# Performance work log

Hardware: AMD Instinct MI355X
Metric: run time of the kernel (lower is better)

## Reference

```python
import jax, jax.numpy as jnp
import numpy as np

SIGMA = 25.0
B = 4096            # number of graphs
N = 1048576         # total nodes across batch
FEAT = 44           # node feature dim
TED = 84            # t_embed_dim = 128 - 44


def setup_inputs() -> dict:
    key = jax.random.key(0)
    ks = jax.random.split(key, 12)
    # ragged graph sizes via sorted random cut points -> ptr of length B+1
    cuts = jnp.sort(jax.random.randint(ks[0], (B - 1,), 0, N))
    ptr = jnp.concatenate([jnp.zeros((1,), jnp.int32), cuts.astype(jnp.int32), jnp.full((1,), N, jnp.int32)])
    node_attr = jax.random.normal(ks[1], (N, FEAT), dtype=jnp.float32)
    t = jax.random.uniform(ks[2], (B,), dtype=jnp.float32, minval=1e-3, maxval=1.0)
    # GaussianFourierProjection buffer (requires_grad=False in torch)
    W_f = jax.random.normal(ks[3], (TED // 2,), dtype=jnp.float32) * 30.0
    # embed Linear 84->84
    embed_w = jax.random.normal(ks[4], (TED, TED), dtype=jnp.float32) / np.sqrt(TED)
    embed_b = jax.random.normal(ks[5], (TED,), dtype=jnp.float32) * 0.01
    # Linear chain 128->64->32->4 (torch convention: W [out, in])
    w0 = jax.random.normal(ks[6], (64, 128), dtype=jnp.float32) / np.sqrt(128)
    b0 = jax.random.normal(ks[7], (64,), dtype=jnp.float32) * 0.01
    w1 = jax.random.normal(ks[8], (32, 64), dtype=jnp.float32) / np.sqrt(64)
    b1 = jax.random.normal(ks[9], (32,), dtype=jnp.float32) * 0.01
    w2 = jax.random.normal(ks[10], (4, 32), dtype=jnp.float32) / np.sqrt(32)
    b2 = jax.random.normal(ks[11], (4,), dtype=jnp.float32) * 0.01
    return {"node_attr": node_attr, "t": t, "ptr": ptr, "W_f": W_f,
            "embed_w": embed_w, "embed_b": embed_b,
            "w0": w0, "b0": b0, "w1": w1, "b1": b1, "w2": w2, "b2": b2}


def reference(node_attr, t, ptr, W_f, embed_w, embed_b, w0, b0, w1, b1, w2, b2):
    swish = lambda x: x * jax.nn.sigmoid(x)
    # GaussianFourierProjection: [B, TED]
    x_proj = t[:, None] * W_f[None, :] * (2.0 * np.pi)
    t_emb = jnp.concatenate([jnp.sin(x_proj), jnp.cos(x_proj)], axis=-1)
    embed = swish(t_emb @ embed_w.T + embed_b)                      # [B, TED]
    # ragged broadcast: graph id per node (replaces the torch per-graph tile loop)
    seg = jnp.searchsorted(ptr, jnp.arange(node_attr.shape[0], dtype=ptr.dtype), side='right') - 1
    h = jnp.concatenate([node_attr, embed[seg]], axis=-1)           # [N, 128]
    h = swish(h @ w0.T + b0)                                        # [N, 64]
    h = swish(h @ w1.T + b1)                                        # [N, 32]
    h = swish(h @ w2.T + b2)                                        # [N, 4]
    std = jnp.sqrt((SIGMA ** (2.0 * t) - 1.0) / (2.0 * np.log(SIGMA)))  # [B]
    return h / std[seg][:, None]
```

## Files before the change

### kernel.cpp

```cpp
#include <hip/hip_runtime.h>
#include <hip/hip_fp16.h>

typedef _Float16 f16x8 __attribute__((ext_vector_type(8)));
typedef __fp16   fp16x2 __attribute__((ext_vector_type(2)));
typedef float f32x4 __attribute__((ext_vector_type(4)));

#define FEAT 44
#define TED  84
#define MT   128
#define WN   32
#define NBLK 768
#define BUFB 6144

__global__ void prep_all(const float* __restrict__ t_arr, const float* __restrict__ W_f,
                         const float* __restrict__ embed_w, const float* __restrict__ embed_b,
                         const float* __restrict__ w0, const float* __restrict__ b0,
                         const float* __restrict__ w1, const float* __restrict__ w2,
                         const int* __restrict__ gptr, int* __restrict__ seg, int do_seg,
                         float* __restrict__ emb0, float* __restrict__ inv_std,
                         _Float16* __restrict__ w0h, _Float16* __restrict__ w1h,
                         _Float16* __restrict__ w2h, int B) {
    int g   = blockIdx.x;
    int tid = threadIdx.x;
    if (g == B) {
        for (int i = tid; i < 64 * 64; i += 128) {
            int o = i >> 6, k = i & 63;
            w0h[i] = (k < FEAT) ? (_Float16)w0[o * 128 + k] : (_Float16)0.f;
        }
        for (int i = tid; i < 32 * 64; i += 128) w1h[i] = (_Float16)w1[i];
        for (int i = tid; i < 16 * 32; i += 128) w2h[i] = (i < 4 * 32) ? (_Float16)w2[i] : (_Float16)0.f;
        return;
    }
    if (do_seg) {
        int a = gptr[g], b = gptr[g + 1];
        for (int i = a + tid; i < b; i += 128) seg[i] = g;
    }
    __shared__ float temb[TED];
    __shared__ float ses[TED];
    float tv = t_arr[g];
    if (tid < TED) {
        int j   = (tid < TED / 2) ? tid : tid - TED / 2;
        float x = tv * W_f[j] * 6.283185307179586f;
        temb[tid] = (tid < TED / 2) ? sinf(x) : cosf(x);
    }
    __syncthreads();
    if (tid < TED) {
        const float* wr = embed_w + tid * TED;
        float s = embed_b[tid];
        #pragma unroll 4
        for (int j = 0; j < TED; ++j) s = fmaf(temb[j], wr[j], s);
        ses[tid] = s / (1.0f + __expf(-s));
    }
    if (tid == TED) {
        const float c = 6.437751649736401f;
        inv_std[g] = rsqrtf(expm1f(c * tv) / c);
    }
    __syncthreads();
    if (tid < 64) {
        const float* wr = w0 + tid * 128 + FEAT;
        float s = b0[tid];
        #pragma unroll 4
        for (int j = 0; j < TED; ++j) s = fmaf(ses[j], wr[j], s);
        emb0[g * 64 + tid] = s;
    }
}

__device__ __forceinline__ float swishf(float x) {
    float e = __builtin_amdgcn_exp2f(x * -1.4426950408889634f);
    return x * __builtin_amdgcn_rcpf(1.0f + e);
}

__device__ __forceinline__ int ubound(const int* __restrict__ p, int n, int v) {
    int lo = 0, hi = n;
    while (lo < hi) { int m = (lo + hi) >> 1; if (p[m] <= v) lo = m + 1; else hi = m; }
    return lo - 1;
}

__device__ __forceinline__ void stage_attr(const float* __restrict__ node_attr, int row0,
                                           const char* lim, char* dst, int lane) {
    const char* g = (const char*)node_attr + (size_t)row0 * (FEAT * 4);
    #pragma unroll
    for (int k = 0; k < 6; ++k) {
        const char* s = g + k * 1024 + lane * 16;
        if (s > lim) s = lim;
        __builtin_amdgcn_global_load_lds(
            (const __attribute__((address_space(1))) unsigned int*)s,
            (__attribute__((address_space(3))) unsigned int*)(dst + k * 1024),
            16, 0, 0);
    }
}

template<bool USE_SEG>
__global__ __launch_bounds__(256)
void scorenet_main(const float* __restrict__ node_attr,
                   const int* __restrict__ gptr, int B,
                   const int* __restrict__ seg_arr,
                   const float* __restrict__ emb0,
                   const float* __restrict__ inv_std_g,
                   const _Float16* __restrict__ w0h,
                   const _Float16* __restrict__ w1h,
                   const _Float16* __restrict__ w2h,
                   const float* __restrict__ b1,
                   const float* __restrict__ b2,
                   float* __restrict__ out, int ntiles, int nbytes_attr) {
    __shared__ __align__(16) char lds[2 * BUFB * 4];

    const int t    = threadIdx.x;
    const int lane = t & 63;
    const int wid  = t >> 6;
    const int lr   = lane & 15;
    const int lk   = lane >> 4;
    const char* lim = (const char*)node_attr + nbytes_attr - 16;

    if (blockIdx.x >= ntiles) return;
    const int stride = gridDim.x;

    f16x8 aw0[2][4];
    #pragma unroll
    for (int kt = 0; kt < 2; ++kt)
        #pragma unroll
        for (int mt = 0; mt < 4; ++mt)
            aw0[kt][mt] = *(const f16x8*)(w0h + (mt * 16 + lr) * 64 + kt * 32 + lk * 8);
    f16x8 aw1[2][2];
    #pragma unroll
    for (int kt = 0; kt < 2; ++kt)
        #pragma unroll
        for (int mt = 0; mt < 2; ++mt)
            aw1[kt][mt] = *(const f16x8*)(w1h + (mt * 16 + lr) * 64 + kt * 32 + lk * 8);
    f16x8 aw2 = *(const f16x8*)(w2h + lr * 32 + lk * 8);
    f32x4 bias1f[2];
    #pragma unroll
    for (int mt = 0; mt < 2; ++mt) {
        float4 bv = *(const float4*)(b1 + mt * 16 + lk * 4);
        bias1f[mt] = f32x4{bv.x, bv.y, bv.z, bv.w};
    }
    float4 b2vv = *(const float4*)b2;
    const f32x4 c2init = (lk == 0) ? f32x4{b2vv.x, b2vv.y, b2vv.z, b2vv.w} : f32x4{0.f, 0.f, 0.f, 0.f};

    char* buf_cur = lds + wid * (2 * BUFB);
    char* buf_nxt = buf_cur + BUFB;

    int tile = blockIdx.x;

    stage_attr(node_attr, tile * MT + wid * WN, lim, buf_cur, lane);
    int s0, s1, n0, n1;
    {
        int wb = tile * MT + wid * WN;
        if (USE_SEG) { s0 = seg_arr[wb + lr]; s1 = seg_arr[wb + 16 + lr]; }
        else { s0 = ubound(gptr, B + 1, wb + lr); s1 = ubound(gptr, B + 1, wb + 16 + lr); }
        int t1 = tile + stride; if (t1 >= ntiles) t1 = tile;
        int wb1 = t1 * MT + wid * WN;
        if (USE_SEG) { n0 = seg_arr[wb1 + lr]; n1 = seg_arr[wb1 + 16 + lr]; }
        else { n0 = ubound(gptr, B + 1, wb1 + lr); n1 = ubound(gptr, B + 1, wb1 + 16 + lr); }
    }

    while (tile < ntiles) {
        const int wb = tile * MT + wid * WN;
        int tp1 = tile + stride;     if (tp1 >= ntiles) tp1 = tile;
        int tp2 = tile + 2 * stride; if (tp2 >= ntiles) tp2 = tile;

        float is0 = inv_std_g[s0];
        float is1 = inv_std_g[s1];
        f32x4 acc0[4][2];
        #pragma unroll
        for (int mt = 0; mt < 4; ++mt) {
            acc0[mt][0] = *(const f32x4*)(emb0 + s0 * 64 + mt * 16 + lk * 4);
            acc0[mt][1] = *(const f32x4*)(emb0 + s1 * 64 + mt * 16 + lk * 4);
        }

        stage_attr(node_attr, tp1 * MT + wid * WN, lim, buf_nxt, lane);

        int m0, m1;
        {
            int wb2 = tp2 * MT + wid * WN;
            if (USE_SEG) { m0 = seg_arr[wb2 + lr]; m1 = seg_arr[wb2 + 16 + lr]; }
            else { m0 = ubound(gptr, B + 1, wb2 + lr); m1 = ubound(gptr, B + 1, wb2 + 16 + lr); }
        }

        asm volatile("s_waitcnt vmcnt(20)" ::: "memory");
        __builtin_amdgcn_sched_barrier(0);

        union u8 { fp16x2 h2[4]; f16x8 v; };
        f16x8 bf[2][2];
        #pragma unroll
        for (int nt = 0; nt < 2; ++nt) {
            const float4* rowp = (const float4*)(buf_cur + (nt * 16 + lr) * (FEAT * 4));
            float4 a = rowp[lk * 2];
            float4 b = rowp[lk * 2 + 1];
            float4 c = make_float4(0.f, 0.f, 0.f, 0.f);
            float4 d = make_float4(0.f, 0.f, 0.f, 0.f);
            if (lk == 0) { c = rowp[8]; d = rowp[9]; }
            else if (lk == 1) { c = rowp[10]; }
            u8 f0, f1;
            f0.h2[0] = __builtin_amdgcn_cvt_pkrtz(a.x, a.y);
            f0.h2[1] = __builtin_amdgcn_cvt_pkrtz(a.z, a.w);
            f0.h2[2] = __builtin_amdgcn_cvt_pkrtz(b.x, b.y);
            f0.h2[3] = __builtin_amdgcn_cvt_pkrtz(b.z, b.w);
            f1.h2[0] = __builtin_amdgcn_cvt_pkrtz(c.x, c.y);
            f1.h2[1] = __builtin_amdgcn_cvt_pkrtz(c.z, c.w);
            f1.h2[2] = __builtin_amdgcn_cvt_pkrtz(d.x, d.y);
            f1.h2[3] = __builtin_amdgcn_cvt_pkrtz(d.z, d.w);
            bf[nt][0] = f0.v;
            bf[nt][1] = f1.v;
        }

        #pragma unroll
        for (int kt = 0; kt < 2; ++kt)
            #pragma unroll
            for (int mt = 0; mt < 4; ++mt)
                #pragma unroll
                for (int nt = 0; nt < 2; ++nt)
                    acc0[mt][nt] = __builtin_amdgcn_mfma_f32_16x16x32_f16(aw0[kt][mt], bf[nt][kt], acc0[mt][nt], 0, 0, 0);

        #pragma unroll
        for (int mt = 0; mt < 4; ++mt)
            #pragma unroll
            for (int nt = 0; nt < 2; ++nt) {
                int j = nt * 16 + lr;
                union { fp16x2 h2[2]; uint2 u; } p;
                p.h2[0] = __builtin_amdgcn_cvt_pkrtz(swishf(acc0[mt][nt][0]), swishf(acc0[mt][nt][1]));
                p.h2[1] = __builtin_amdgcn_cvt_pkrtz(swishf(acc0[mt][nt][2]), swishf(acc0[mt][nt][3]));
                int addr = j * 128 + (mt * 16 + lk * 4) * 2;
                *(uint2*)(buf_cur + (addr ^ ((j & 7) << 4))) = p.u;
            }

        f32x4 acc1[2][2];
        #pragma unroll
        for (int mt = 0; mt < 2; ++mt) { acc1[mt][0] = bias1f[mt]; acc1[mt][1] = bias1f[mt]; }
        #pragma unroll
        for (int kt = 0; kt < 2; ++kt) {
            f16x8 bx[2];
            #pragma unroll
            for (int nt = 0; nt < 2; ++nt) {
                int j    = nt * 16 + lr;
                int addr = j * 128 + kt * 64 + lk * 16;
                bx[nt] = *(const f16x8*)(buf_cur + (addr ^ ((j & 7) << 4)));
            }
            #pragma unroll
            for (int mt = 0; mt < 2; ++mt)
                #pragma unroll
                for (int nt = 0; nt < 2; ++nt)
                    acc1[mt][nt] = __builtin_amdgcn_mfma_f32_16x16x32_f16(aw1[kt][mt], bx[nt], acc1[mt][nt], 0, 0, 0);
        }

        #pragma unroll
        for (int mt = 0; mt < 2; ++mt)
            #pragma unroll
            for (int nt = 0; nt < 2; ++nt) {
                int j = nt * 16 + lr;
                union { fp16x2 h2[2]; uint2 u; } p;
                p.h2[0] = __builtin_amdgcn_cvt_pkrtz(swishf(acc1[mt][nt][0]), swishf(acc1[mt][nt][1]));
                p.h2[1] = __builtin_amdgcn_cvt_pkrtz(swishf(acc1[mt][nt][2]), swishf(acc1[mt][nt][3]));
                int addr = 4096 + j * 64 + (mt * 16 + lk * 4) * 2;
                *(uint2*)(buf_cur + (addr ^ ((j & 3) << 4))) = p.u;
            }

        f32x4 acc2[2] = {c2init, c2init};
        #pragma unroll
        for (int nt = 0; nt < 2; ++nt) {
            int j    = nt * 16 + lr;
            int addr = 4096 + j * 64 + lk * 16;
            f16x8 bx = *(const f16x8*)(buf_cur + (addr ^ ((j & 3) << 4)));
            acc2[nt] = __builtin_amdgcn_mfma_f32_16x16x32_f16(aw2, bx, acc2[nt], 0, 0, 0);
        }
        if (lk == 0) {
            #pragma unroll
            for (int nt = 0; nt < 2; ++nt) {
                int j = nt * 16 + lr;
                float is = nt ? is1 : is0;
                float4 o;
                o.x = swishf(acc2[nt][0]) * is;
                o.y = swishf(acc2[nt][1]) * is;
                o.z = swishf(acc2[nt][2]) * is;
                o.w = swishf(acc2[nt][3]) * is;
                *(float4*)(out + (size_t)(wb + j) * 4) = o;
            }
        }

        { char* tmp = buf_cur; buf_cur = buf_nxt; buf_nxt = tmp; }
        s0 = n0; s1 = n1; n0 = m0; n1 = m1;
        tile += stride;
    }
}

extern "C" void kernel_launch(void* const* d_in, const int* in_sizes, int n_in,
                              void* d_out, int out_size, void* d_ws, size_t ws_size,
                              hipStream_t stream) {
    const float* node_attr = (const float*)d_in[0];
    const float* t_arr     = (const float*)d_in[1];
    const int*   gptr      = (const int*)d_in[2];
    const float* W_f       = (const float*)d_in[3];
    const float* embed_w   = (const float*)d_in[4];
    const float* embed_b   = (const float*)d_in[5];
    const float* w0        = (const float*)d_in[6];
    const float* b0        = (const float*)d_in[7];
    const float* w1        = (const float*)d_in[8];
    const float* b1        = (const float*)d_in[9];
    const float* w2        = (const float*)d_in[10];
    const float* b2        = (const float*)d_in[11];
    float* out = (float*)d_out;

    const int N = in_sizes[0] / FEAT;
    const int B = in_sizes[2] - 1;
    const int ntiles = N / MT;
    const int nbytes_attr = in_sizes[0] * 4;

    char* ws = (char*)d_ws;
    size_t off = 0;
    float*    emb0    = (float*)(ws + off); off += (size_t)B * 64 * sizeof(float);
    off = (off + 1023) & ~(size_t)1023;
    float*    inv_std = (float*)(ws + off); off += (size_t)B * sizeof(float);
    off = (off + 1023) & ~(size_t)1023;
    _Float16* w0h = (_Float16*)(ws + off);  off += 64 * 64 * sizeof(_Float16);
    _Float16* w1h = (_Float16*)(ws + off);  off += 32 * 64 * sizeof(_Float16);
    _Float16* w2h = (_Float16*)(ws + off);  off += 16 * 32 * sizeof(_Float16);
    off = (off + 1023) & ~(size_t)1023;
    int* seg = (int*)(ws + off);
    size_t need_with_seg = off + (size_t)N * sizeof(int);
    bool use_seg = (ws_size >= need_with_seg);

    const int grid = (ntiles < NBLK) ? ntiles : NBLK;

    prep_all<<<B + 1, 128, 0, stream>>>(t_arr, W_f, embed_w, embed_b, w0, b0, w1, w2,
                                        gptr, seg, use_seg ? 1 : 0,
                                        emb0, inv_std, w0h, w1h, w2h, B);
    if (use_seg) {
        scorenet_main<true><<<grid, 256, 0, stream>>>(node_attr, gptr, B, seg, emb0, inv_std,
                                                      w0h, w1h, w2h, b1, b2, out, ntiles, nbytes_attr);
    } else {
        scorenet_main<false><<<grid, 256, 0, stream>>>(node_attr, gptr, B, seg, emb0, inv_std,
                                                       w0h, w1h, w2h, b1, b2, out, ntiles, nbytes_attr);
    }
}
```

Before: 83.83 us.

## Batch prep over 16 graphs with LDS-staged weights; pair swish reciprocals

```diff
diff --git a/kernel.cpp b/kernel.cpp
--- a/kernel.cpp
+++ b/kernel.cpp
@@ -11,63 +11,103 @@
 #define WN   32
 #define NBLK 768
 #define BUFB 6144
-
-__global__ void prep_all(const float* __restrict__ t_arr, const float* __restrict__ W_f,
-                         const float* __restrict__ embed_w, const float* __restrict__ embed_b,
-                         const float* __restrict__ w0, const float* __restrict__ b0,
-                         const float* __restrict__ w1, const float* __restrict__ w2,
-                         const int* __restrict__ gptr, int* __restrict__ seg, int do_seg,
-                         float* __restrict__ emb0, float* __restrict__ inv_std,
-                         _Float16* __restrict__ w0h, _Float16* __restrict__ w1h,
-                         _Float16* __restrict__ w2h, int B) {
-    int g   = blockIdx.x;
+#define GPB  16
+
+__global__ __launch_bounds__(256)
+void prep_blocked(const float* __restrict__ t_arr, const float* __restrict__ W_f,
+                  const float* __restrict__ embed_w, const float* __restrict__ embed_b,
+                  const float* __restrict__ w0, const float* __restrict__ b0,
+                  const float* __restrict__ w1, const float* __restrict__ w2,
+                  const int* __restrict__ gptr, int* __restrict__ seg, int do_seg,
+                  float* __restrict__ emb0, float* __restrict__ inv_std,
+                  _Float16* __restrict__ w0h, _Float16* __restrict__ w1h,
+                  _Float16* __restrict__ w2h, int B) {
     int tid = threadIdx.x;
-    if (g == B) {
-        for (int i = tid; i < 64 * 64; i += 128) {
+    if (blockIdx.x == gridDim.x - 1) {
+        for (int i = tid; i < 64 * 64; i += 256) {
             int o = i >> 6, k = i & 63;
             w0h[i] = (k < FEAT) ? (_Float16)w0[o * 128 + k] : (_Float16)0.f;
         }
-        for (int i = tid; i < 32 * 64; i += 128) w1h[i] = (_Float16)w1[i];
-        for (int i = tid; i < 16 * 32; i += 128) w2h[i] = (i < 4 * 32) ? (_Float16)w2[i] : (_Float16)0.f;
+        for (int i = tid; i < 32 * 64; i += 256) w1h[i] = (_Float16)w1[i];
+        for (int i = tid; i < 16 * 32; i += 256) w2h[i] = (i < 4 * 32) ? (_Float16)w2[i] : (_Float16)0.f;
         return;
     }
+    __shared__ float ew[TED * 85];
+    __shared__ float w0p[64 * 85];
+    __shared__ float temb[2][TED];
+    __shared__ float ses[2][TED];
+
+    const int g0 = blockIdx.x * GPB;
+
+    for (int i = tid; i < TED * TED; i += 256) {
+        int o = i / TED, j = i - o * TED;
+        ew[o * 85 + j] = embed_w[i];
+    }
+    for (int i = tid; i < 64 * TED; i += 256) {
+        int o = i / TED, j = i - o * TED;
+        w0p[o * 85 + j] = w0[o * 128 + FEAT + j];
+    }
+
     if (do_seg) {
-        int a = gptr[g], b = gptr[g + 1];
-        for (int i = a + tid; i < b; i += 128) seg[i] = g;
-    }
-    __shared__ float temb[TED];
-    __shared__ float ses[TED];
-    float tv = t_arr[g];
-    if (tid < TED) {
-        int j   = (tid < TED / 2) ? tid : tid - TED / 2;
-        float x = tv * W_f[j] * 6.283185307179586f;
-        temb[tid] = (tid < TED / 2) ? sinf(x) : cosf(x);
+        for (int g = g0; g < g0 + GPB && g < B; ++g) {
+            int a = gptr[g], b = gptr[g + 1];
+            for (int i = a + tid; i < b; i += 256) seg[i] = g;
+        }
     }
     __syncthreads();
-    if (tid < TED) {
-        const float* wr = embed_w + tid * TED;
-        float s = embed_b[tid];
-        #pragma unroll 4
-        for (int j = 0; j < TED; ++j) s = fmaf(temb[j], wr[j], s);
-        ses[tid] = s / (1.0f + __expf(-s));
-    }
-    if (tid == TED) {
-        const float c = 6.437751649736401f;
-        inv_std[g] = rsqrtf(expm1f(c * tv) / c);
-    }
-    __syncthreads();
-    if (tid < 64) {
-        const float* wr = w0 + tid * 128 + FEAT;
-        float s = b0[tid];
-        #pragma unroll 4
-        for (int j = 0; j < TED; ++j) s = fmaf(ses[j], wr[j], s);
-        emb0[g * 64 + tid] = s;
-    }
-}
-
-__device__ __forceinline__ float swishf(float x) {
-    float e = __builtin_amdgcn_exp2f(x * -1.4426950408889634f);
-    return x * __builtin_amdgcn_rcpf(1.0f + e);
+
+    const int sub  = tid >> 7;
+    const int tid2 = tid & 127;
+
+    for (int p = 0; p < GPB / 2; ++p) {
+        int g = g0 + p * 2 + sub;
+        bool ok = (g < B);
+        float tv = ok ? t_arr[g] : 0.f;
+        if (ok && tid2 < TED) {
+            int j   = (tid2 < TED / 2) ? tid2 : tid2 - TED / 2;
+            float x = tv * W_f[j] * 6.283185307179586f;
+            temb[sub][tid2] = (tid2 < TED / 2) ? sinf(x) : cosf(x);
+        }
+        __syncthreads();
+        if (ok && tid2 < TED) {
+            const float* wr = ew + tid2 * 85;
+            float s = embed_b[tid2];
+            #pragma unroll 4
+            for (int j = 0; j < TED; ++j) s = fmaf(temb[sub][j], wr[j], s);
+            ses[sub][tid2] = s / (1.0f + __expf(-s));
+        }
+        if (ok && tid2 == TED) {
+            const float c = 6.437751649736401f;
+            inv_std[g] = rsqrtf(expm1f(c * tv) / c);
+        }
+        __syncthreads();
+        if (ok && tid2 < 64) {
+            const float* wr = w0p + tid2 * 85;
+            float s = b0[tid2];
+            #pragma unroll 4
+            for (int j = 0; j < TED; ++j) s = fmaf(ses[sub][j], wr[j], s);
+            emb0[g * 64 + tid2] = s;
+        }
+        __syncthreads();
+    }
+}
+
+__device__ __forceinline__ fp16x2 swish_pair_h(float x0, float x1) {
+    const float c = -1.4426950408889634f;
+    float e0 = __builtin_amdgcn_exp2f(x0 * c);
+    float e1 = __builtin_amdgcn_exp2f(x1 * c);
+    float a = 1.0f + e0, b = 1.0f + e1;
+    float inv = __builtin_amdgcn_rcpf(a * b);
+    return __builtin_amdgcn_cvt_pkrtz(x0 * (b * inv), x1 * (a * inv));
+}
+__device__ __forceinline__ void swish_pair_f(float x0, float x1, float& r0, float& r1) {
+    const float c = -1.4426950408889634f;
+    float e0 = __builtin_amdgcn_exp2f(x0 * c);
+    float e1 = __builtin_amdgcn_exp2f(x1 * c);
+    float a = 1.0f + e0, b = 1.0f + e1;
+    float inv = __builtin_amdgcn_rcpf(a * b);
+    r0 = x0 * (b * inv);
+    r1 = x1 * (a * inv);
 }
 
 __device__ __forceinline__ int ubound(const int* __restrict__ p, int n, int v) {
@@ -218,8 +258,8 @@
             for (int nt = 0; nt < 2; ++nt) {
                 int j = nt * 16 + lr;
                 union { fp16x2 h2[2]; uint2 u; } p;
-                p.h2[0] = __builtin_amdgcn_cvt_pkrtz(swishf(acc0[mt][nt][0]), swishf(acc0[mt][nt][1]));
-                p.h2[1] = __builtin_amdgcn_cvt_pkrtz(swishf(acc0[mt][nt][2]), swishf(acc0[mt][nt][3]));
+                p.h2[0] = swish_pair_h(acc0[mt][nt][0], acc0[mt][nt][1]);
+                p.h2[1] = swish_pair_h(acc0[mt][nt][2], acc0[mt][nt][3]);
                 int addr = j * 128 + (mt * 16 + lk * 4) * 2;
                 *(uint2*)(buf_cur + (addr ^ ((j & 7) << 4))) = p.u;
             }
@@ -249,8 +289,8 @@
             for (int nt = 0; nt < 2; ++nt) {
                 int j = nt * 16 + lr;
                 union { fp16x2 h2[2]; uint2 u; } p;
-                p.h2[0] = __builtin_amdgcn_cvt_pkrtz(swishf(acc1[mt][nt][0]), swishf(acc1[mt][nt][1]));
-                p.h2[1] = __builtin_amdgcn_cvt_pkrtz(swishf(acc1[mt][nt][2]), swishf(acc1[mt][nt][3]));
+                p.h2[0] = swish_pair_h(acc1[mt][nt][0], acc1[mt][nt][1]);
+                p.h2[1] = swish_pair_h(acc1[mt][nt][2], acc1[mt][nt][3]);
                 int addr = 4096 + j * 64 + (mt * 16 + lk * 4) * 2;
                 *(uint2*)(buf_cur + (addr ^ ((j & 3) << 4))) = p.u;
             }
@@ -269,10 +309,9 @@
                 int j = nt * 16 + lr;
                 float is = nt ? is1 : is0;
                 float4 o;
-                o.x = swishf(acc2[nt][0]) * is;
-                o.y = swishf(acc2[nt][1]) * is;
-                o.z = swishf(acc2[nt][2]) * is;
-                o.w = swishf(acc2[nt][3]) * is;
+                swish_pair_f(acc2[nt][0], acc2[nt][1], o.x, o.y);
+                swish_pair_f(acc2[nt][2], acc2[nt][3], o.z, o.w);
+                o.x *= is; o.y *= is; o.z *= is; o.w *= is;
                 *(float4*)(out + (size_t)(wb + j) * 4) = o;
             }
         }
@@ -320,10 +359,11 @@
     bool use_seg = (ws_size >= need_with_seg);
 
     const int grid = (ntiles < NBLK) ? ntiles : NBLK;
-
-    prep_all<<<B + 1, 128, 0, stream>>>(t_arr, W_f, embed_w, embed_b, w0, b0, w1, w2,
-                                        gptr, seg, use_seg ? 1 : 0,
-                                        emb0, inv_std, w0h, w1h, w2h, B);
+    const int prep_blocks = (B + GPB - 1) / GPB + 1;
+
+    prep_blocked<<<prep_blocks, 256, 0, stream>>>(t_arr, W_f, embed_w, embed_b, w0, b0, w1, w2,
+                                                  gptr, seg, use_seg ? 1 : 0,
+                                                  emb0, inv_std, w0h, w1h, w2h, B);
     if (use_seg) {
         scorenet_main<true><<<grid, 256, 0, stream>>>(node_attr, gptr, B, seg, emb0, inv_std,
                                                       w0h, w1h, w2h, b1, b2, out, ntiles, nbytes_attr);
```

Result: slower. 85.81 us (+2.4%).

## Software-pipeline layer-0 MFMA with previous tile's back layers

Applied to the files above, without the earlier changes.

```diff
diff --git a/kernel.cpp b/kernel.cpp
--- a/kernel.cpp
+++ b/kernel.cpp
@@ -9,8 +9,10 @@
 #define TED  84
 #define MT   128
 #define WN   32
-#define NBLK 768
+#define NBLK 512
 #define BUFB 6144
+#define WSLICE 16384
+#define WORK_OFF 12288
 
 __global__ void prep_all(const float* __restrict__ t_arr, const float* __restrict__ W_f,
                          const float* __restrict__ embed_w, const float* __restrict__ embed_b,
@@ -90,6 +92,74 @@
     }
 }
 
+__device__ __forceinline__ void back_half(const f32x4 (*accp)[2], float isp0, float isp1,
+                                          int wbp, char* work, float* __restrict__ out,
+                                          const f16x8 (*aw1)[2], f16x8 aw2,
+                                          const f32x4* bias1f, f32x4 c2init,
+                                          int lr, int lk) {
+    #pragma unroll
+    for (int mt = 0; mt < 4; ++mt)
+        #pragma unroll
+        for (int nt = 0; nt < 2; ++nt) {
+            int j = nt * 16 + lr;
+            union { fp16x2 h2[2]; uint2 u; } p;
+            p.h2[0] = __builtin_amdgcn_cvt_pkrtz(swishf(accp[mt][nt][0]), swishf(accp[mt][nt][1]));
+            p.h2[1] = __builtin_amdgcn_cvt_pkrtz(swishf(accp[mt][nt][2]), swishf(accp[mt][nt][3]));
+            int addr = j * 128 + (mt * 16 + lk * 4) * 2;
+            *(uint2*)(work + (addr ^ ((j & 7) << 4))) = p.u;
+        }
+    f32x4 acc1[2][2];
+    #pragma unroll
+    for (int mt = 0; mt < 2; ++mt) { acc1[mt][0] = bias1f[mt]; acc1[mt][1] = bias1f[mt]; }
+    #pragma unroll
+    for (int kt = 0; kt < 2; ++kt) {
+        f16x8 bx[2];
+        #pragma unroll
+        for (int nt = 0; nt < 2; ++nt) {
+            int j    = nt * 16 + lr;
+            int addr = j * 128 + kt * 64 + lk * 16;
+            bx[nt] = *(const f16x8*)(work + (addr ^ ((j & 7) << 4)));
+        }
+        #pragma unroll
+        for (int mt = 0; mt < 2; ++mt)
+            #pragma unroll
+            for (int nt = 0; nt < 2; ++nt)
+                acc1[mt][nt] = __builtin_amdgcn_mfma_f32_16x16x32_f16(aw1[kt][mt], bx[nt], acc1[mt][nt], 0, 0, 0);
+    }
+    #pragma unroll
+    for (int mt = 0; mt < 2; ++mt)
+        #pragma unroll
+        for (int nt = 0; nt < 2; ++nt) {
+            int j = nt * 16 + lr;
+            union { fp16x2 h2[2]; uint2 u; } p;
+            p.h2[0] = __builtin_amdgcn_cvt_pkrtz(swishf(acc1[mt][nt][0]), swishf(acc1[mt][nt][1]));
+            p.h2[1] = __builtin_amdgcn_cvt_pkrtz(swishf(acc1[mt][nt][2]), swishf(acc1[mt][nt][3]));
+            int addr = j * 64 + (mt * 16 + lk * 4) * 2;
+            *(uint2*)(work + (addr ^ ((j & 3) << 4))) = p.u;
+        }
+    f32x4 acc2[2] = {c2init, c2init};
+    #pragma unroll
+    for (int nt = 0; nt < 2; ++nt) {
+        int j    = nt * 16 + lr;
+        int addr = j * 64 + lk * 16;
+        f16x8 bx = *(const f16x8*)(work + (addr ^ ((j & 3) << 4)));
+        acc2[nt] = __builtin_amdgcn_mfma_f32_16x16x32_f16(aw2, bx, acc2[nt], 0, 0, 0);
+    }
+    if (lk == 0) {
+        #pragma unroll
+        for (int nt = 0; nt < 2; ++nt) {
+            int j = nt * 16 + lr;
+            float is = nt ? isp1 : isp0;
+            float4 o;
+            o.x = swishf(acc2[nt][0]) * is;
+            o.y = swishf(acc2[nt][1]) * is;
+            o.z = swishf(acc2[nt][2]) * is;
+            o.w = swishf(acc2[nt][3]) * is;
+            *(float4*)(out + (size_t)(wbp + j) * 4) = o;
+        }
+    }
+}
+
 template<bool USE_SEG>
 __global__ __launch_bounds__(256)
 void scorenet_main(const float* __restrict__ node_attr,
@@ -103,7 +173,7 @@
                    const float* __restrict__ b1,
                    const float* __restrict__ b2,
                    float* __restrict__ out, int ntiles, int nbytes_attr) {
-    __shared__ __align__(16) char lds[2 * BUFB * 4];
+    __shared__ __align__(16) char lds[65536];
 
     const int t    = threadIdx.x;
     const int lane = t & 63;
@@ -137,8 +207,10 @@
     float4 b2vv = *(const float4*)b2;
     const f32x4 c2init = (lk == 0) ? f32x4{b2vv.x, b2vv.y, b2vv.z, b2vv.w} : f32x4{0.f, 0.f, 0.f, 0.f};
 
-    char* buf_cur = lds + wid * (2 * BUFB);
-    char* buf_nxt = buf_cur + BUFB;
+    char* base    = lds + wid * WSLICE;
+    char* buf_cur = base;
+    char* buf_nxt = base + BUFB;
+    char* const work = base + WORK_OFF;
 
     int tile = blockIdx.x;
 
@@ -154,30 +226,29 @@
         else { n0 = ubound(gptr, B + 1, wb1 + lr); n1 = ubound(gptr, B + 1, wb1 + 16 + lr); }
     }
 
-    while (tile < ntiles) {
-        const int wb = tile * MT + wid * WN;
-        int tp1 = tile + stride;     if (tp1 >= ntiles) tp1 = tile;
-        int tp2 = tile + 2 * stride; if (tp2 >= ntiles) tp2 = tile;
-
-        float is0 = inv_std_g[s0];
-        float is1 = inv_std_g[s1];
-        f32x4 acc0[4][2];
+    f32x4 acc_p[4][2];
+    float isp0, isp1;
+    int wbp;
+
+    {
+        wbp  = tile * MT + wid * WN;
+        isp0 = inv_std_g[s0];
+        isp1 = inv_std_g[s1];
         #pragma unroll
         for (int mt = 0; mt < 4; ++mt) {
-            acc0[mt][0] = *(const f32x4*)(emb0 + s0 * 64 + mt * 16 + lk * 4);
-            acc0[mt][1] = *(const f32x4*)(emb0 + s1 * 64 + mt * 16 + lk * 4);
-        }
-
-        stage_attr(node_attr, tp1 * MT + wid * WN, lim, buf_nxt, lane);
-
+            acc_p[mt][0] = *(const f32x4*)(emb0 + s0 * 64 + mt * 16 + lk * 4);
+            acc_p[mt][1] = *(const f32x4*)(emb0 + s1 * 64 + mt * 16 + lk * 4);
+        }
+        int t1 = tile + stride;     if (t1 >= ntiles) t1 = tile;
+        stage_attr(node_attr, t1 * MT + wid * WN, lim, buf_nxt, lane);
+        int t2 = tile + 2 * stride; if (t2 >= ntiles) t2 = tile;
+        int wb2 = t2 * MT + wid * WN;
         int m0, m1;
-        {
-            int wb2 = tp2 * MT + wid * WN;
-            if (USE_SEG) { m0 = seg_arr[wb2 + lr]; m1 = seg_arr[wb2 + 16 + lr]; }
-            else { m0 = ubound(gptr, B + 1, wb2 + lr); m1 = ubound(gptr, B + 1, wb2 + 16 + lr); }
-        }
-
-        asm volatile("s_waitcnt vmcnt(20)" ::: "memory");
+        if (USE_SEG) { m0 = seg_arr[wb2 + lr]; m1 = seg_arr[wb2 + 16 + lr]; }
+        else { m0 = ubound(gptr, B + 1, wb2 + lr); m1 = ubound(gptr, B + 1, wb2 + 16 + lr); }
+
+        if (USE_SEG) { asm volatile("s_waitcnt vmcnt(22)" ::: "memory"); }
+        else         { asm volatile("s_waitcnt vmcnt(0)"  ::: "memory"); }
         __builtin_amdgcn_sched_barrier(0);
 
         union u8 { fp16x2 h2[4]; f16x8 v; };
@@ -203,84 +274,86 @@
             bf[nt][0] = f0.v;
             bf[nt][1] = f1.v;
         }
-
         #pragma unroll
         for (int kt = 0; kt < 2; ++kt)
             #pragma unroll
             for (int mt = 0; mt < 4; ++mt)
                 #pragma unroll
                 for (int nt = 0; nt < 2; ++nt)
-                    acc0[mt][nt] = __builtin_amdgcn_mfma_f32_16x16x32_f16(aw0[kt][mt], bf[nt][kt], acc0[mt][nt], 0, 0, 0);
-
-        #pragma unroll
-        for (int mt = 0; mt < 4; ++mt)
+                    acc_p[mt][nt] = __builtin_amdgcn_mfma_f32_16x16x32_f16(aw0[kt][mt], bf[nt][kt], acc_p[mt][nt], 0, 0, 0);
+
+        s0 = n0; s1 = n1; n0 = m0; n1 = m1;
+        { char* tmp = buf_cur; buf_cur = buf_nxt; buf_nxt = tmp; }
+        tile += stride;
+    }
+
+    while (tile < ntiles) {
+        const int wb = tile * MT + wid * WN;
+
+        float isc0 = inv_std_g[s0];
+        float isc1 = inv_std_g[s1];
+        f32x4 accC[4][2];
+        #pragma unroll
+        for (int mt = 0; mt < 4; ++mt) {
+            accC[mt][0] = *(const f32x4*)(emb0 + s0 * 64 + mt * 16 + lk * 4);
+            accC[mt][1] = *(const f32x4*)(emb0 + s1 * 64 + mt * 16 + lk * 4);
+        }
+
+        int t1 = tile + stride;     if (t1 >= ntiles) t1 = tile;
+        stage_attr(node_attr, t1 * MT + wid * WN, lim, buf_nxt, lane);
+
+        int t2 = tile + 2 * stride; if (t2 >= ntiles) t2 = tile;
+        int wb2 = t2 * MT + wid * WN;
+        int m0, m1;
+        if (USE_SEG) { m0 = seg_arr[wb2 + lr]; m1 = seg_arr[wb2 + 16 + lr]; }
+        else { m0 = ubound(gptr, B + 1, wb2 + lr); m1 = ubound(gptr, B + 1, wb2 + 16 + lr); }
+
+        back_half(acc_p, isp0, isp1, wbp, work, out, aw1, aw2, bias1f, c2init, lr, lk);
+
+        if (USE_SEG) { asm volatile("s_waitcnt vmcnt(22)" ::: "memory"); }
+        else         { asm volatile("s_waitcnt vmcnt(0)"  ::: "memory"); }
+        __builtin_amdgcn_sched_barrier(0);
+
+        union u8 { fp16x2 h2[4]; f16x8 v; };
+        f16x8 bf[2][2];
+        #pragma unroll
+        for (int nt = 0; nt < 2; ++nt) {
+            const float4* rowp = (const float4*)(buf_cur + (nt * 16 + lr) * (FEAT * 4));
+            float4 a = rowp[lk * 2];
+            float4 b = rowp[lk * 2 + 1];
+            float4 c = make_float4(0.f, 0.f, 0.f, 0.f);
+            float4 d = make_float4(0.f, 0.f, 0.f, 0.f);
+            if (lk == 0) { c = rowp[8]; d = rowp[9]; }
+            else if (lk == 1) { c = rowp[10]; }
+            u8 f0, f1;
+            f0.h2[0] = __builtin_amdgcn_cvt_pkrtz(a.x, a.y);
+            f0.h2[1] = __builtin_amdgcn_cvt_pkrtz(a.z, a.w);
+            f0.h2[2] = __builtin_amdgcn_cvt_pkrtz(b.x, b.y);
+            f0.h2[3] = __builtin_amdgcn_cvt_pkrtz(b.z, b.w);
+            f1.h2[0] = __builtin_amdgcn_cvt_pkrtz(c.x, c.y);
+            f1.h2[1] = __builtin_amdgcn_cvt_pkrtz(c.z, c.w);
+            f1.h2[2] = __builtin_amdgcn_cvt_pkrtz(d.x, d.y);
+            f1.h2[3] = __builtin_amdgcn_cvt_pkrtz(d.z, d.w);
+            bf[nt][0] = f0.v;
+            bf[nt][1] = f1.v;
+        }
+        #pragma unroll
+        for (int kt = 0; kt < 2; ++kt)
             #pragma unroll
-            for (int nt = 0; nt < 2; ++nt) {
-                int j = nt * 16 + lr;
-                union { fp16x2 h2[2]; uint2 u; } p;
-                p.h2[0] = __builtin_amdgcn_cvt_pkrtz(swishf(acc0[mt][nt][0]), swishf(acc0[mt][nt][1]));
-                p.h2[1] = __builtin_amdgcn_cvt_pkrtz(swishf(acc0[mt][nt][2]), swishf(acc0[mt][nt][3]));
-                int addr = j * 128 + (mt * 16 + lk * 4) * 2;
-                *(uint2*)(buf_cur + (addr ^ ((j & 7) << 4))) = p.u;
-            }
-
-        f32x4 acc1[2][2];
-        #pragma unroll
-        for (int mt = 0; mt < 2; ++mt) { acc1[mt][0] = bias1f[mt]; acc1[mt][1] = bias1f[mt]; }
-        #pragma unroll
-        for (int kt = 0; kt < 2; ++kt) {
-            f16x8 bx[2];
-            #pragma unroll
-            for (int nt = 0; nt < 2; ++nt) {
-                int j    = nt * 16 + lr;
-                int addr = j * 128 + kt * 64 + lk * 16;
-                bx[nt] = *(const f16x8*)(buf_cur + (addr ^ ((j & 7) << 4)));
-            }
-            #pragma unroll
-            for (int mt = 0; mt < 2; ++mt)
+            for (int mt = 0; mt < 4; ++mt)
                 #pragma unroll
                 for (int nt = 0; nt < 2; ++nt)
-                    acc1[mt][nt] = __builtin_amdgcn_mfma_f32_16x16x32_f16(aw1[kt][mt], bx[nt], acc1[mt][nt], 0, 0, 0);
-        }
-
-        #pragma unroll
-        for (int mt = 0; mt < 2; ++mt)
-            #pragma unroll
-            for (int nt = 0; nt < 2; ++nt) {
-                int j = nt * 16 + lr;
-                union { fp16x2 h2[2]; uint2 u; } p;
-                p.h2[0] = __builtin_amdgcn_cvt_pkrtz(swishf(acc1[mt][nt][0]), swishf(acc1[mt][nt][1]));
-                p.h2[1] = __builtin_amdgcn_cvt_pkrtz(swishf(acc1[mt][nt][2]), swishf(acc1[mt][nt][3]));
-                int addr = 4096 + j * 64 + (mt * 16 + lk * 4) * 2;
-                *(uint2*)(buf_cur + (addr ^ ((j & 3) << 4))) = p.u;
-            }
-
-        f32x4 acc2[2] = {c2init, c2init};
-        #pragma unroll
-        for (int nt = 0; nt < 2; ++nt) {
-            int j    = nt * 16 + lr;
-            int addr = 4096 + j * 64 + lk * 16;
-            f16x8 bx = *(const f16x8*)(buf_cur + (addr ^ ((j & 3) << 4)));
-            acc2[nt] = __builtin_amdgcn_mfma_f32_16x16x32_f16(aw2, bx, acc2[nt], 0, 0, 0);
-        }
-        if (lk == 0) {
-            #pragma unroll
-            for (int nt = 0; nt < 2; ++nt) {
-                int j = nt * 16 + lr;
-                float is = nt ? is1 : is0;
-                float4 o;
-                o.x = swishf(acc2[nt][0]) * is;
-                o.y = swishf(acc2[nt][1]) * is;
-                o.z = swishf(acc2[nt][2]) * is;
-                o.w = swishf(acc2[nt][3]) * is;
-                *(float4*)(out + (size_t)(wb + j) * 4) = o;
-            }
-        }
-
+                    accC[mt][nt] = __builtin_amdgcn_mfma_f32_16x16x32_f16(aw0[kt][mt], bf[nt][kt], accC[mt][nt], 0, 0, 0);
+
+        #pragma unroll
+        for (int mt = 0; mt < 4; ++mt) { acc_p[mt][0] = accC[mt][0]; acc_p[mt][1] = accC[mt][1]; }
+        isp0 = isc0; isp1 = isc1; wbp = wb;
+        s0 = n0; s1 = n1; n0 = m0; n1 = m1;
         { char* tmp = buf_cur; buf_cur = buf_nxt; buf_nxt = tmp; }
-        s0 = n0; s1 = n1; n0 = m0; n1 = m1;
         tile += stride;
     }
+
+    back_half(acc_p, isp0, isp1, wbp, work, out, aw1, aw2, bias1f, c2init, lr, lk);
 }
 
 extern "C" void kernel_launch(void* const* d_in, const int* in_sizes, int n_in,
```

Result: slower. 85.61 us (+2.1%).

## Fuse prep and main kernels into one cooperative launch with grid sync

Applied to the files above, without the earlier changes.

```diff
diff --git a/kernel.cpp b/kernel.cpp
--- a/kernel.cpp
+++ b/kernel.cpp
@@ -1,5 +1,8 @@
 #include <hip/hip_runtime.h>
 #include <hip/hip_fp16.h>
+#include <hip/hip_cooperative_groups.h>
+
+namespace cg = cooperative_groups;
 
 typedef _Float16 f16x8 __attribute__((ext_vector_type(8)));
 typedef __fp16   fp16x2 __attribute__((ext_vector_type(2)));
@@ -12,68 +15,9 @@
 #define NBLK 768
 #define BUFB 6144
 
-__global__ void prep_all(const float* __restrict__ t_arr, const float* __restrict__ W_f,
-                         const float* __restrict__ embed_w, const float* __restrict__ embed_b,
-                         const float* __restrict__ w0, const float* __restrict__ b0,
-                         const float* __restrict__ w1, const float* __restrict__ w2,
-                         const int* __restrict__ gptr, int* __restrict__ seg, int do_seg,
-                         float* __restrict__ emb0, float* __restrict__ inv_std,
-                         _Float16* __restrict__ w0h, _Float16* __restrict__ w1h,
-                         _Float16* __restrict__ w2h, int B) {
-    int g   = blockIdx.x;
-    int tid = threadIdx.x;
-    if (g == B) {
-        for (int i = tid; i < 64 * 64; i += 128) {
-            int o = i >> 6, k = i & 63;
-            w0h[i] = (k < FEAT) ? (_Float16)w0[o * 128 + k] : (_Float16)0.f;
-        }
-        for (int i = tid; i < 32 * 64; i += 128) w1h[i] = (_Float16)w1[i];
-        for (int i = tid; i < 16 * 32; i += 128) w2h[i] = (i < 4 * 32) ? (_Float16)w2[i] : (_Float16)0.f;
-        return;
-    }
-    if (do_seg) {
-        int a = gptr[g], b = gptr[g + 1];
-        for (int i = a + tid; i < b; i += 128) seg[i] = g;
-    }
-    __shared__ float temb[TED];
-    __shared__ float ses[TED];
-    float tv = t_arr[g];
-    if (tid < TED) {
-        int j   = (tid < TED / 2) ? tid : tid - TED / 2;
-        float x = tv * W_f[j] * 6.283185307179586f;
-        temb[tid] = (tid < TED / 2) ? sinf(x) : cosf(x);
-    }
-    __syncthreads();
-    if (tid < TED) {
-        const float* wr = embed_w + tid * TED;
-        float s = embed_b[tid];
-        #pragma unroll 4
-        for (int j = 0; j < TED; ++j) s = fmaf(temb[j], wr[j], s);
-        ses[tid] = s / (1.0f + __expf(-s));
-    }
-    if (tid == TED) {
-        const float c = 6.437751649736401f;
-        inv_std[g] = rsqrtf(expm1f(c * tv) / c);
-    }
-    __syncthreads();
-    if (tid < 64) {
-        const float* wr = w0 + tid * 128 + FEAT;
-        float s = b0[tid];
-        #pragma unroll 4
-        for (int j = 0; j < TED; ++j) s = fmaf(ses[j], wr[j], s);
-        emb0[g * 64 + tid] = s;
-    }
-}
-
 __device__ __forceinline__ float swishf(float x) {
     float e = __builtin_amdgcn_exp2f(x * -1.4426950408889634f);
     return x * __builtin_amdgcn_rcpf(1.0f + e);
-}
-
-__device__ __forceinline__ int ubound(const int* __restrict__ p, int n, int v) {
-    int lo = 0, hi = n;
-    while (lo < hi) { int m = (lo + hi) >> 1; if (p[m] <= v) lo = m + 1; else hi = m; }
-    return lo - 1;
 }
 
 __device__ __forceinline__ void stage_attr(const float* __restrict__ node_attr, int row0,
@@ -82,7 +26,7 @@
     #pragma unroll
     for (int k = 0; k < 6; ++k) {
         const char* s = g + k * 1024 + lane * 16;
-        if (s > lim) s = lim;
+        if (k == 5 && s > lim) s = lim;
         __builtin_amdgcn_global_load_lds(
             (const __attribute__((address_space(1))) unsigned int*)s,
             (__attribute__((address_space(3))) unsigned int*)(dst + k * 1024),
@@ -90,29 +34,87 @@
     }
 }
 
-template<bool USE_SEG>
-__global__ __launch_bounds__(256)
-void scorenet_main(const float* __restrict__ node_attr,
+__global__ __launch_bounds__(256, 3)
+void scorenet_coop(const float* __restrict__ node_attr,
                    const int* __restrict__ gptr, int B,
-                   const int* __restrict__ seg_arr,
-                   const float* __restrict__ emb0,
-                   const float* __restrict__ inv_std_g,
-                   const _Float16* __restrict__ w0h,
-                   const _Float16* __restrict__ w1h,
-                   const _Float16* __restrict__ w2h,
+                   const float* __restrict__ t_arr,
+                   const float* __restrict__ W_f,
+                   const float* __restrict__ embed_w,
+                   const float* __restrict__ embed_b,
+                   const float* __restrict__ w0,
+                   const float* __restrict__ b0,
+                   const float* __restrict__ w1,
                    const float* __restrict__ b1,
+                   const float* __restrict__ w2,
                    const float* __restrict__ b2,
+                   int* __restrict__ seg,
+                   float* __restrict__ emb0,
+                   float* __restrict__ inv_std,
+                   _Float16* __restrict__ w0h,
+                   _Float16* __restrict__ w1h,
+                   _Float16* __restrict__ w2h,
                    float* __restrict__ out, int ntiles, int nbytes_attr) {
-    __shared__ __align__(16) char lds[2 * BUFB * 4];
+    __shared__ __align__(16) char lds[49152];
 
     const int t    = threadIdx.x;
     const int lane = t & 63;
     const int wid  = t >> 6;
     const int lr   = lane & 15;
     const int lk   = lane >> 4;
+
+    if (blockIdx.x == 0) {
+        for (int i = t; i < 64 * 64; i += 256) {
+            int o = i >> 6, k = i & 63;
+            w0h[i] = (k < FEAT) ? (_Float16)w0[o * 128 + k] : (_Float16)0.f;
+        }
+        for (int i = t; i < 32 * 64; i += 256) w1h[i] = (_Float16)w1[i];
+        for (int i = t; i < 16 * 32; i += 256) w2h[i] = (i < 4 * 32) ? (_Float16)w2[i] : (_Float16)0.f;
+    }
+    {
+        float* temb = (float*)lds;
+        float* ses  = temb + 2 * TED;
+        const int sub  = t >> 7;
+        const int tid2 = t & 127;
+        for (int g0 = blockIdx.x * 2; g0 < B; g0 += gridDim.x * 2) {
+            int g = g0 + sub;
+            bool ok = (g < B);
+            float tv = ok ? t_arr[g] : 0.f;
+            if (ok) {
+                int a = gptr[g], b = gptr[g + 1];
+                for (int i = a + tid2; i < b; i += 128) seg[i] = g;
+            }
+            if (ok && tid2 < TED) {
+                int j   = (tid2 < TED / 2) ? tid2 : tid2 - TED / 2;
+                float x = tv * W_f[j] * 6.283185307179586f;
+                temb[sub * TED + tid2] = (tid2 < TED / 2) ? sinf(x) : cosf(x);
+            }
+            __syncthreads();
+            if (ok && tid2 < TED) {
+                const float* wr = embed_w + tid2 * TED;
+                float s = embed_b[tid2];
+                #pragma unroll 4
+                for (int j = 0; j < TED; ++j) s = fmaf(temb[sub * TED + j], wr[j], s);
+                ses[sub * TED + tid2] = s / (1.0f + __expf(-s));
+            }
+            if (ok && tid2 == TED) {
+                const float c = 6.437751649736401f;
+                inv_std[g] = rsqrtf(expm1f(c * tv) / c);
+            }
+            __syncthreads();
+            if (ok && tid2 < 64) {
+                const float* wr = w0 + tid2 * 128 + FEAT;
+                float s = b0[tid2];
+                #pragma unroll 4
+                for (int j = 0; j < TED; ++j) s = fmaf(ses[sub * TED + j], wr[j], s);
+                emb0[g * 64 + tid2] = s;
+            }
+            __syncthreads();
+        }
+    }
+    __threadfence();
+    cg::this_grid().sync();
+
     const char* lim = (const char*)node_attr + nbytes_attr - 16;
-
-    if (blockIdx.x >= ntiles) return;
     const int stride = gridDim.x;
 
     f16x8 aw0[2][4];
@@ -141,145 +143,143 @@
     char* buf_nxt = buf_cur + BUFB;
 
     int tile = blockIdx.x;
-
-    stage_attr(node_attr, tile * MT + wid * WN, lim, buf_cur, lane);
-    int s0, s1, n0, n1;
-    {
-        int wb = tile * MT + wid * WN;
-        if (USE_SEG) { s0 = seg_arr[wb + lr]; s1 = seg_arr[wb + 16 + lr]; }
-        else { s0 = ubound(gptr, B + 1, wb + lr); s1 = ubound(gptr, B + 1, wb + 16 + lr); }
-        int t1 = tile + stride; if (t1 >= ntiles) t1 = tile;
-        int wb1 = t1 * MT + wid * WN;
-        if (USE_SEG) { n0 = seg_arr[wb1 + lr]; n1 = seg_arr[wb1 + 16 + lr]; }
-        else { n0 = ubound(gptr, B + 1, wb1 + lr); n1 = ubound(gptr, B + 1, wb1 + 16 + lr); }
-    }
-
-    while (tile < ntiles) {
-        const int wb = tile * MT + wid * WN;
-        int tp1 = tile + stride;     if (tp1 >= ntiles) tp1 = tile;
-        int tp2 = tile + 2 * stride; if (tp2 >= ntiles) tp2 = tile;
-
-        float is0 = inv_std_g[s0];
-        float is1 = inv_std_g[s1];
-        f32x4 acc0[4][2];
-        #pragma unroll
-        for (int mt = 0; mt < 4; ++mt) {
-            acc0[mt][0] = *(const f32x4*)(emb0 + s0 * 64 + mt * 16 + lk * 4);
-            acc0[mt][1] = *(const f32x4*)(emb0 + s1 * 64 + mt * 16 + lk * 4);
+    if (tile < ntiles) {
+        stage_attr(node_attr, tile * MT + wid * WN, lim, buf_cur, lane);
+        int s0, s1, n0, n1;
+        {
+            int wb = tile * MT + wid * WN;
+            s0 = seg[wb + lr]; s1 = seg[wb + 16 + lr];
+            int t1 = tile + stride; if (t1 >= ntiles) t1 = tile;
+            int wb1 = t1 * MT + wid * WN;
+            n0 = seg[wb1 + lr]; n1 = seg[wb1 + 16 + lr];
         }
 
-        stage_attr(node_attr, tp1 * MT + wid * WN, lim, buf_nxt, lane);
-
-        int m0, m1;
-        {
-            int wb2 = tp2 * MT + wid * WN;
-            if (USE_SEG) { m0 = seg_arr[wb2 + lr]; m1 = seg_arr[wb2 + 16 + lr]; }
-            else { m0 = ubound(gptr, B + 1, wb2 + lr); m1 = ubound(gptr, B + 1, wb2 + 16 + lr); }
-        }
-
-        asm volatile("s_waitcnt vmcnt(20)" ::: "memory");
-        __builtin_amdgcn_sched_barrier(0);
-
-        union u8 { fp16x2 h2[4]; f16x8 v; };
-        f16x8 bf[2][2];
-        #pragma unroll
-        for (int nt = 0; nt < 2; ++nt) {
-            const float4* rowp = (const float4*)(buf_cur + (nt * 16 + lr) * (FEAT * 4));
-            float4 a = rowp[lk * 2];
-            float4 b = rowp[lk * 2 + 1];
-            float4 c = make_float4(0.f, 0.f, 0.f, 0.f);
-            float4 d = make_float4(0.f, 0.f, 0.f, 0.f);
-            if (lk == 0) { c = rowp[8]; d = rowp[9]; }
-            else if (lk == 1) { c = rowp[10]; }
-            u8 f0, f1;
-            f0.h2[0] = __builtin_amdgcn_cvt_pkrtz(a.x, a.y);
-            f0.h2[1] = __builtin_amdgcn_cvt_pkrtz(a.z, a.w);
-            f0.h2[2] = __builtin_amdgcn_cvt_pkrtz(b.x, b.y);
-            f0.h2[3] = __builtin_amdgcn_cvt_pkrtz(b.z, b.w);
-            f1.h2[0] = __builtin_amdgcn_cvt_pkrtz(c.x, c.y);
-            f1.h2[1] = __builtin_amdgcn_cvt_pkrtz(c.z, c.w);
-            f1.h2[2] = __builtin_amdgcn_cvt_pkrtz(d.x, d.y);
-            f1.h2[3] = __builtin_amdgcn_cvt_pkrtz(d.z, d.w);
-            bf[nt][0] = f0.v;
-            bf[nt][1] = f1.v;
-        }
-
-        #pragma unroll
-        for (int kt = 0; kt < 2; ++kt)
+        while (tile < ntiles) {
+            const int wb = tile * MT + wid * WN;
+            int tp1 = tile + stride;     if (tp1 >= ntiles) tp1 = tile;
+            int tp2 = tile + 2 * stride; if (tp2 >= ntiles) tp2 = tile;
+
+            float is0 = inv_std[s0];
+            float is1 = inv_std[s1];
+            f32x4 acc0[4][2];
+            #pragma unroll
+            for (int mt = 0; mt < 4; ++mt) {
+                acc0[mt][0] = *(const f32x4*)(emb0 + s0 * 64 + mt * 16 + lk * 4);
+                acc0[mt][1] = *(const f32x4*)(emb0 + s1 * 64 + mt * 16 + lk * 4);
+            }
+
+            stage_attr(node_attr, tp1 * MT + wid * WN, lim, buf_nxt, lane);
+
+            int m0, m1;
+            {
+                int wb2 = tp2 * MT + wid * WN;
+                m0 = seg[wb2 + lr]; m1 = seg[wb2 + 16 + lr];
+            }
+
+            asm volatile("s_waitcnt vmcnt(20)" ::: "memory");
+            __builtin_amdgcn_sched_barrier(0);
+
+            union u8 { fp16x2 h2[4]; f16x8 v; };
+            f16x8 bf[2][2];
+            #pragma unroll
+            for (int nt = 0; nt < 2; ++nt) {
+                const float4* rowp = (const float4*)(buf_cur + (nt * 16 + lr) * (FEAT * 4));
+                float4 a = rowp[lk * 2];
+                float4 b = rowp[lk * 2 + 1];
+                float4 c = make_float4(0.f, 0.f, 0.f, 0.f);
+                float4 d = make_float4(0.f, 0.f, 0.f, 0.f);
+                if (lk == 0) { c = rowp[8]; d = rowp[9]; }
+                else if (lk == 1) { c = rowp[10]; }
+                u8 f0, f1;
+                f0.h2[0] = __builtin_amdgcn_cvt_pkrtz(a.x, a.y);
+                f0.h2[1] = __builtin_amdgcn_cvt_pkrtz(a.z, a.w);
+                f0.h2[2] = __builtin_amdgcn_cvt_pkrtz(b.x, b.y);
+                f0.h2[3] = __builtin_amdgcn_cvt_pkrtz(b.z, b.w);
+                f1.h2[0] = __builtin_amdgcn_cvt_pkrtz(c.x, c.y);
+                f1.h2[1] = __builtin_amdgcn_cvt_pkrtz(c.z, c.w);
+                f1.h2[2] = __builtin_amdgcn_cvt_pkrtz(d.x, d.y);
+                f1.h2[3] = __builtin_amdgcn_cvt_pkrtz(d.z, d.w);
+                bf[nt][0] = f0.v;
+                bf[nt][1] = f1.v;
+            }
+
+            #pragma unroll
+            for (int kt = 0; kt < 2; ++kt)
+                #pragma unroll
+                for (int mt = 0; mt < 4; ++mt)
+                    #pragma unroll
+                    for (int nt = 0; nt < 2; ++nt)
+                        acc0[mt][nt] = __builtin_amdgcn_mfma_f32_16x16x32_f16(aw0[kt][mt], bf[nt][kt], acc0[mt][nt], 0, 0, 0);
+
             #pragma unroll
             for (int mt = 0; mt < 4; ++mt)
                 #pragma unroll
-                for (int nt = 0; nt < 2; ++nt)
-                    acc0[mt][nt] = __builtin_amdgcn_mfma_f32_16x16x32_f16(aw0[kt][mt], bf[nt][kt], acc0[mt][nt], 0, 0, 0);
-
-        #pragma unroll
-        for (int mt = 0; mt < 4; ++mt)
-            #pragma unroll
-            for (int nt = 0; nt < 2; ++nt) {
-                int j = nt * 16 + lr;
-                union { fp16x2 h2[2]; uint2 u; } p;
-                p.h2[0] = __builtin_amdgcn_cvt_pkrtz(swishf(acc0[mt][nt][0]), swishf(acc0[mt][nt][1]));
-                p.h2[1] = __builtin_amdgcn_cvt_pkrtz(swishf(acc0[mt][nt][2]), swishf(acc0[mt][nt][3]));
-                int addr = j * 128 + (mt * 16 + lk * 4) * 2;
-                *(uint2*)(buf_cur + (addr ^ ((j & 7) << 4))) = p.u;
-            }
-
-        f32x4 acc1[2][2];
-        #pragma unroll
-        for (int mt = 0; mt < 2; ++mt) { acc1[mt][0] = bias1f[mt]; acc1[mt][1] = bias1f[mt]; }
-        #pragma unroll
-        for (int kt = 0; kt < 2; ++kt) {
-            f16x8 bx[2];
+                for (int nt = 0; nt < 2; ++nt) {
+                    int j = nt * 16 + lr;
+                    union { fp16x2 h2[2]; uint2 u; } p;
+                    p.h2[0] = __builtin_amdgcn_cvt_pkrtz(swishf(acc0[mt][nt][0]), swishf(acc0[mt][nt][1]));
+                    p.h2[1] = __builtin_amdgcn_cvt_pkrtz(swishf(acc0[mt][nt][2]), swishf(acc0[mt][nt][3]));
+                    int addr = j * 128 + (mt * 16 + lk * 4) * 2;
+                    *(uint2*)(buf_cur + (addr ^ ((j & 7) << 4))) = p.u;
+                }
+
+            f32x4 acc1[2][2];
+            #pragma unroll
+            for (int mt = 0; mt < 2; ++mt) { acc1[mt][0] = bias1f[mt]; acc1[mt][1] = bias1f[mt]; }
+            #pragma unroll
+            for (int kt = 0; kt < 2; ++kt) {
+                f16x8 bx[2];
+                #pragma unroll
+                for (int nt = 0; nt < 2; ++nt) {
+                    int j    = nt * 16 + lr;
+                    int addr = j * 128 + kt * 64 + lk * 16;
+                    bx[nt] = *(const f16x8*)(buf_cur + (addr ^ ((j & 7) << 4)));
+                }
+                #pragma unroll
+                for (int mt = 0; mt < 2; ++mt)
+                    #pragma unroll
+                    for (int nt = 0; nt < 2; ++nt)
+                        acc1[mt][nt] = __builtin_amdgcn_mfma_f32_16x16x32_f16(aw1[kt][mt], bx[nt], acc1[mt][nt], 0, 0, 0);
+            }
+
+            #pragma unroll
+            for (int mt = 0; mt < 2; ++mt)
+                #pragma unroll
+                for (int nt = 0; nt < 2; ++nt) {
+                    int j = nt * 16 + lr;
+                    union { fp16x2 h2[2]; uint2 u; } p;
+                    p.h2[0] = __builtin_amdgcn_cvt_pkrtz(swishf(acc1[mt][nt][0]), swishf(acc1[mt][nt][1]));
+                    p.h2[1] = __builtin_amdgcn_cvt_pkrtz(swishf(acc1[mt][nt][2]), swishf(acc1[mt][nt][3]));
+                    int addr = 4096 + j * 64 + (mt * 16 + lk * 4) * 2;
+                    *(uint2*)(buf_cur + (addr ^ ((j & 3) << 4))) = p.u;
+                }
+
+            f32x4 acc2[2] = {c2init, c2init};
             #pragma unroll
             for (int nt = 0; nt < 2; ++nt) {
                 int j    = nt * 16 + lr;
-                int addr = j * 128 + kt * 64 + lk * 16;
-                bx[nt] = *(const f16x8*)(buf_cur + (addr ^ ((j & 7) << 4)));
-            }
-            #pragma unroll
-            for (int mt = 0; mt < 2; ++mt)
-                #pragma unroll
-                for (int nt = 0; nt < 2; ++nt)
-                    acc1[mt][nt] = __builtin_amdgcn_mfma_f32_16x16x32_f16(aw1[kt][mt], bx[nt], acc1[mt][nt], 0, 0, 0);
+                int addr = 4096 + j * 64 + lk * 16;
+                f16x8 bx = *(const f16x8*)(buf_cur + (addr ^ ((j & 3) << 4)));
+                acc2[nt] = __builtin_amdgcn_mfma_f32_16x16x32_f16(aw2, bx, acc2[nt], 0, 0, 0);
+            }
+            if (lk == 0) {
+                #pragma unroll
+                for (int nt = 0; nt < 2; ++nt) {
+                    int j = nt * 16 + lr;
+                    float is = nt ? is1 : is0;
+                    float4 o;
+                    o.x = swishf(acc2[nt][0]) * is;
+                    o.y = swishf(acc2[nt][1]) * is;
+                    o.z = swishf(acc2[nt][2]) * is;
+                    o.w = swishf(acc2[nt][3]) * is;
+                    *(float4*)(out + (size_t)(wb + j) * 4) = o;
+                }
+            }
+
+            { char* tmp = buf_cur; buf_cur = buf_nxt; buf_nxt = tmp; }
+            s0 = n0; s1 = n1; n0 = m0; n1 = m1;
+            tile += stride;
         }
-
-        #pragma unroll
-        for (int mt = 0; mt < 2; ++mt)
-            #pragma unroll
-            for (int nt = 0; nt < 2; ++nt) {
-                int j = nt * 16 + lr;
-                union { fp16x2 h2[2]; uint2 u; } p;
-                p.h2[0] = __builtin_amdgcn_cvt_pkrtz(swishf(acc1[mt][nt][0]), swishf(acc1[mt][nt][1]));
-                p.h2[1] = __builtin_amdgcn_cvt_pkrtz(swishf(acc1[mt][nt][2]), swishf(acc1[mt][nt][3]));
-                int addr = 4096 + j * 64 + (mt * 16 + lk * 4) * 2;
-                *(uint2*)(buf_cur + (addr ^ ((j & 3) << 4))) = p.u;
-            }
-
-        f32x4 acc2[2] = {c2init, c2init};
-        #pragma unroll
-        for (int nt = 0; nt < 2; ++nt) {
-            int j    = nt * 16 + lr;
-            int addr = 4096 + j * 64 + lk * 16;
-            f16x8 bx = *(const f16x8*)(buf_cur + (addr ^ ((j & 3) << 4)));
-            acc2[nt] = __builtin_amdgcn_mfma_f32_16x16x32_f16(aw2, bx, acc2[nt], 0, 0, 0);
-        }
-        if (lk == 0) {
-            #pragma unroll
-            for (int nt = 0; nt < 2; ++nt) {
-                int j = nt * 16 + lr;
-                float is = nt ? is1 : is0;
-                float4 o;
-                o.x = swishf(acc2[nt][0]) * is;
-                o.y = swishf(acc2[nt][1]) * is;
-                o.z = swishf(acc2[nt][2]) * is;
-                o.w = swishf(acc2[nt][3]) * is;
-                *(float4*)(out + (size_t)(wb + j) * 4) = o;
-            }
-        }
-
-        { char* tmp = buf_cur; buf_cur = buf_nxt; buf_nxt = tmp; }
-        s0 = n0; s1 = n1; n0 = m0; n1 = m1;
-        tile += stride;
     }
 }
 
@@ -301,9 +301,9 @@
     float* out = (float*)d_out;
 
     const int N = in_sizes[0] / FEAT;
-    const int B = in_sizes[2] - 1;
+    int B = in_sizes[2] - 1;
     const int ntiles = N / MT;
-    const int nbytes_attr = in_sizes[0] * 4;
+    int nbytes_attr = in_sizes[0] * 4;
 
     char* ws = (char*)d_ws;
     size_t off = 0;
@@ -316,19 +316,23 @@
     _Float16* w2h = (_Float16*)(ws + off);  off += 16 * 32 * sizeof(_Float16);
     off = (off + 1023) & ~(size_t)1023;
     int* seg = (int*)(ws + off);
-    size_t need_with_seg = off + (size_t)N * sizeof(int);
-    bool use_seg = (ws_size >= need_with_seg);
-
-    const int grid = (ntiles < NBLK) ? ntiles : NBLK;
-
-    prep_all<<<B + 1, 128, 0, stream>>>(t_arr, W_f, embed_w, embed_b, w0, b0, w1, w2,
-                                        gptr, seg, use_seg ? 1 : 0,
-                                        emb0, inv_std, w0h, w1h, w2h, B);
-    if (use_seg) {
-        scorenet_main<true><<<grid, 256, 0, stream>>>(node_attr, gptr, B, seg, emb0, inv_std,
-                                                      w0h, w1h, w2h, b1, b2, out, ntiles, nbytes_attr);
-    } else {
-        scorenet_main<false><<<grid, 256, 0, stream>>>(node_attr, gptr, B, seg, emb0, inv_std,
-                                                       w0h, w1h, w2h, b1, b2, out, ntiles, nbytes_attr);
-    }
+
+    int occ = 0;
+    hipOccupancyMaxActiveBlocksPerMultiprocessor(&occ, (const void*)scorenet_coop, 256, 0);
+    if (occ < 1) occ = 1;
+    int grid = occ * 256;
+    if (grid > NBLK) grid = NBLK;
+    if (grid > ntiles) grid = ntiles;
+
+    int nt_ = ntiles;
+    void* args[] = {
+        (void*)&node_attr, (void*)&gptr, (void*)&B,
+        (void*)&t_arr, (void*)&W_f, (void*)&embed_w, (void*)&embed_b,
+        (void*)&w0, (void*)&b0, (void*)&w1, (void*)&b1, (void*)&w2, (void*)&b2,
+        (void*)&seg, (void*)&emb0, (void*)&inv_std,
+        (void*)&w0h, (void*)&w1h, (void*)&w2h,
+        (void*)&out, (void*)&nt_, (void*)&nbytes_attr
+    };
+    hipLaunchCooperativeKernel((const void*)scorenet_coop, dim3(grid), dim3(256),
+                               args, 0, stream);
 }
```

New measurement: 184.0 us. 120% more time.
